# Optimization experiments

Hardware: AMD Instinct MI355X
Metric: run time of the kernel (lower is better)

## Reference

```python
import jax, jax.numpy as jnp
import numpy as np

N, W, D, IC, OC, R = 256, 1, 64, 32, 32, 8


def setup_inputs() -> dict:
    key = jax.random.key(0)
    k1, k2 = jax.random.split(key)
    x = jax.random.normal(k1, (N, W, D, IC, R), dtype=jnp.float32)
    weights = jax.random.normal(k2, (D, IC, OC, R), dtype=jnp.float32)
    return {"x": x, "weights": weights}


def reference(x, weights):
    # x: [n, w, d, ic, r] -> [n, w, d, ic, 1, r]
    # weights: [d, ic, oc, r] -> broadcast as [1, 1, d, ic, oc, r]
    # out: logsumexp over ic -> [n, w, d, oc, r]
    logits = x[:, :, :, :, None, :] + weights[None, None]
    return jax.nn.logsumexp(logits, axis=3)
```

## Files before the change

### kernel.cpp

```cpp
#include <hip/hip_runtime.h>
#include <hip/hip_bf16.h>


typedef __attribute__((ext_vector_type(8))) short bf16x8;
typedef __attribute__((ext_vector_type(4))) float f32x4;

constexpr int kD = 64, kIC = 32, kOC = 32, kR = 8;

__device__ __forceinline__ unsigned pk2(float a, float b) {
    __hip_bfloat162 h = __float22bfloat162_rn(make_float2(a, b));
    unsigned r;
    __builtin_memcpy(&r, &h, 4);
    return r;
}

__global__ __launch_bounds__(256) void lse_kernel(
    const float* __restrict__ x, const float* __restrict__ w,
    float* __restrict__ out)
{
    __shared__ __align__(16) unsigned short wsm[2 * 8 * 64 * 8];
    __shared__ __align__(16) unsigned short xs [8 * 64 * 8];

    const int t  = threadIdx.x;
    const int d  = blockIdx.x;
    const int n0 = blockIdx.y * 16;

    const int cw = t & 7, chw = cw & 1, cqw = cw >> 1, ol = t >> 3;
    const float* wd = w + (size_t)d * (kIC * kOC * kR);
    float4 wv[8];
    #pragma unroll
    for (int a = 0; a < 4; ++a) {
        const int ic0 = 8 * a + 2 * cqw;
        wv[2*a]   = *reinterpret_cast<const float4*>(wd + (size_t)ic0 * 256 + ol * 8 + 4 * chw);
        wv[2*a+1] = *reinterpret_cast<const float4*>(wd + (size_t)(ic0 + 1) * 256 + ol * 8 + 4 * chw);
    }

    const int cx = t & 15, e = cx & 1, icp = cx >> 1, nlx = t >> 4;
    const float* xr = x + (size_t)(n0 + nlx) * (kD * kIC * kR) + (size_t)d * (kIC * kR);
    float4 xv[4];
    #pragma unroll
    for (int a = 0; a < 2; ++a) {
        const int ic0 = 16 * a + 2 * icp;
        xv[2*a]   = *reinterpret_cast<const float4*>(xr + ic0 * 8 + 4 * e);
        xv[2*a+1] = *reinterpret_cast<const float4*>(xr + ic0 * 8 + 8 + 4 * e);
    }

    {
        const int col = ol & 15, u = ol >> 4, s0 = 2 * cqw;
        #pragma unroll
        for (int a = 0; a < 4; ++a)
            #pragma unroll
            for (int j = 0; j < 4; ++j) {
                const int r = 4 * chw + j;
                const unsigned pk = pk2(
                    __expf(reinterpret_cast<const float*>(&wv[2*a])[j]),
                    __expf(reinterpret_cast<const float*>(&wv[2*a+1])[j]));
                *reinterpret_cast<unsigned*>(&wsm[((u * 8 + r) * 64 + a * 16 + col) * 8 + s0]) = pk;
            }
    }

    {
        const int ig_lo = icp >> 2;
        const int s0x = 2 * (icp & 3);
        #pragma unroll
        for (int a = 0; a < 2; ++a) {
            const int lane = (2 * a + ig_lo) * 16 + nlx;
            #pragma unroll
            for (int j = 0; j < 4; ++j) {
                const int r = 4 * e + j;
                const unsigned pk = pk2(
                    __expf(reinterpret_cast<const float*>(&xv[2*a])[j]),
                    __expf(reinterpret_cast<const float*>(&xv[2*a+1])[j]));
                *reinterpret_cast<unsigned*>(&xs[(r * 64 + lane) * 8 + s0x]) = pk;
            }
        }
    }

    __syncthreads();

    const int wave = t >> 6;
    const int wu  = wave & 1;
    const int wrh = wave >> 1;
    const int l   = t & 63;
    const int colL = l & 15, qL = l >> 4;

    f32x4 acc[4];
    #pragma unroll
    for (int j = 0; j < 4; ++j) {
        const int r = wrh * 4 + j;
        bf16x8 av = *reinterpret_cast<const bf16x8*>(&xs [(r * 64 + l) * 8]);
        bf16x8 bv = *reinterpret_cast<const bf16x8*>(&wsm[((wu * 8 + r) * 64 + l) * 8]);
        f32x4 z = {0.f, 0.f, 0.f, 0.f};
        acc[j] = __builtin_amdgcn_mfma_f32_16x16x32_bf16(av, bv, z, 0, 0, 0);
    }

    #pragma unroll
    for (int i = 0; i < 4; ++i) {
        const int n = n0 + qL * 4 + i;
        float4 v;
        v.x = __logf(acc[0][i]); v.y = __logf(acc[1][i]);
        v.z = __logf(acc[2][i]); v.w = __logf(acc[3][i]);
        *reinterpret_cast<float4*>(out + (size_t)n * (kD * kOC * kR)
            + (size_t)d * (kOC * kR) + (size_t)(wu * 16 + colL) * 8 + wrh * 4) = v;
    }
}

extern "C" void kernel_launch(void* const* d_in, const int* in_sizes, int n_in,
                              void* d_out, int out_size, void* d_ws, size_t ws_size,
                              hipStream_t stream) {
    const float* x = (const float*)d_in[0];
    const float* w = (const float*)d_in[1];
    float* out = (float*)d_out;
    dim3 grid(kD, 16);
    lse_kernel<<<grid, 256, 0, stream>>>(x, w, out);
}
```

Measured before the change: 12.75 us.

## Process two batch tiles per block, reusing staged weights and overlapping staging

Each block now covers 32 batch rows (two 16-row tiles) rather than 16, so the exp-transformed weight tile in shared memory is built once and used twice, and the grid is halved to 512 blocks. The second x tile is exponentiated and staged into a second shared buffer while the first tile's MFMA results are turned into logs and stored, giving some overlap. In exchange it needs more registers and shared memory per block and has fewer blocks to spread across the 256 CUs.

```diff
diff --git a/kernel.cpp b/kernel.cpp
--- a/kernel.cpp
+++ b/kernel.cpp
@@ -19,11 +19,12 @@
     float* __restrict__ out)
 {
     __shared__ __align__(16) unsigned short wsm[2 * 8 * 64 * 8];
-    __shared__ __align__(16) unsigned short xs [8 * 64 * 8];
+    __shared__ __align__(16) unsigned short xs [2 * 8 * 64 * 8];
 
     const int t  = threadIdx.x;
-    const int d  = blockIdx.x;
-    const int n0 = blockIdx.y * 16;
+    const int d  = blockIdx.x >> 3;
+    const int pp = blockIdx.x & 7;
+    const int n0 = pp * 32;
 
     const int cw = t & 7, chw = cw & 1, cqw = cw >> 1, ol = t >> 3;
     const float* wd = w + (size_t)d * (kIC * kOC * kR);
@@ -36,13 +37,16 @@
     }
 
     const int cx = t & 15, e = cx & 1, icp = cx >> 1, nlx = t >> 4;
-    const float* xr = x + (size_t)(n0 + nlx) * (kD * kIC * kR) + (size_t)d * (kIC * kR);
-    float4 xv[4];
+    const float* xr0 = x + (size_t)(n0 + nlx) * (kD * kIC * kR) + (size_t)d * (kIC * kR);
+    const float* xr1 = xr0 + (size_t)16 * (kD * kIC * kR);
+    float4 x0v[4], x1v[4];
     #pragma unroll
     for (int a = 0; a < 2; ++a) {
         const int ic0 = 16 * a + 2 * icp;
-        xv[2*a]   = *reinterpret_cast<const float4*>(xr + ic0 * 8 + 4 * e);
-        xv[2*a+1] = *reinterpret_cast<const float4*>(xr + ic0 * 8 + 8 + 4 * e);
+        x0v[2*a]   = *reinterpret_cast<const float4*>(xr0 + ic0 * 8 + 4 * e);
+        x0v[2*a+1] = *reinterpret_cast<const float4*>(xr0 + ic0 * 8 + 8 + 4 * e);
+        x1v[2*a]   = *reinterpret_cast<const float4*>(xr1 + ic0 * 8 + 4 * e);
+        x1v[2*a+1] = *reinterpret_cast<const float4*>(xr1 + ic0 * 8 + 8 + 4 * e);
     }
 
     {
@@ -59,9 +63,8 @@
             }
     }
 
-    {
-        const int ig_lo = icp >> 2;
-        const int s0x = 2 * (icp & 3);
+    const int ig_lo = icp >> 2, s0x = 2 * (icp & 3);
+    auto stage_x = [&](int buf, const float4* xcv) {
         #pragma unroll
         for (int a = 0; a < 2; ++a) {
             const int lane = (2 * a + ig_lo) * 16 + nlx;
@@ -69,13 +72,14 @@
             for (int j = 0; j < 4; ++j) {
                 const int r = 4 * e + j;
                 const unsigned pk = pk2(
-                    __expf(reinterpret_cast<const float*>(&xv[2*a])[j]),
-                    __expf(reinterpret_cast<const float*>(&xv[2*a+1])[j]));
-                *reinterpret_cast<unsigned*>(&xs[(r * 64 + lane) * 8 + s0x]) = pk;
+                    __expf(reinterpret_cast<const float*>(&xcv[2*a])[j]),
+                    __expf(reinterpret_cast<const float*>(&xcv[2*a+1])[j]));
+                *reinterpret_cast<unsigned*>(&xs[((buf * 8 + r) * 64 + lane) * 8 + s0x]) = pk;
             }
         }
-    }
+    };
 
+    stage_x(0, x0v);
     __syncthreads();
 
     const int wave = t >> 6;
@@ -84,25 +88,35 @@
     const int l   = t & 63;
     const int colL = l & 15, qL = l >> 4;
 
-    f32x4 acc[4];
-    #pragma unroll
-    for (int j = 0; j < 4; ++j) {
-        const int r = wrh * 4 + j;
-        bf16x8 av = *reinterpret_cast<const bf16x8*>(&xs [(r * 64 + l) * 8]);
-        bf16x8 bv = *reinterpret_cast<const bf16x8*>(&wsm[((wu * 8 + r) * 64 + l) * 8]);
-        f32x4 z = {0.f, 0.f, 0.f, 0.f};
-        acc[j] = __builtin_amdgcn_mfma_f32_16x16x32_bf16(av, bv, z, 0, 0, 0);
-    }
+    auto compute = [&](int buf, f32x4* acc) {
+        #pragma unroll
+        for (int j = 0; j < 4; ++j) {
+            const int r = wrh * 4 + j;
+            bf16x8 av = *reinterpret_cast<const bf16x8*>(&xs [((buf * 8 + r) * 64 + l) * 8]);
+            bf16x8 bv = *reinterpret_cast<const bf16x8*>(&wsm[((wu * 8 + r) * 64 + l) * 8]);
+            f32x4 z = {0.f, 0.f, 0.f, 0.f};
+            acc[j] = __builtin_amdgcn_mfma_f32_16x16x32_bf16(av, bv, z, 0, 0, 0);
+        }
+    };
+    auto logstore = [&](int nt0, const f32x4* acc) {
+        #pragma unroll
+        for (int i = 0; i < 4; ++i) {
+            const int n = nt0 + qL * 4 + i;
+            float4 v;
+            v.x = __logf(acc[0][i]); v.y = __logf(acc[1][i]);
+            v.z = __logf(acc[2][i]); v.w = __logf(acc[3][i]);
+            *reinterpret_cast<float4*>(out + (size_t)n * (kD * kOC * kR)
+                + (size_t)d * (kOC * kR) + (size_t)(wu * 16 + colL) * 8 + wrh * 4) = v;
+        }
+    };
 
-    #pragma unroll
-    for (int i = 0; i < 4; ++i) {
-        const int n = n0 + qL * 4 + i;
-        float4 v;
-        v.x = __logf(acc[0][i]); v.y = __logf(acc[1][i]);
-        v.z = __logf(acc[2][i]); v.w = __logf(acc[3][i]);
-        *reinterpret_cast<float4*>(out + (size_t)n * (kD * kOC * kR)
-            + (size_t)d * (kOC * kR) + (size_t)(wu * 16 + colL) * 8 + wrh * 4) = v;
-    }
+    f32x4 acc0[4], acc1[4];
+    compute(0, acc0);
+    stage_x(1, x1v);
+    logstore(n0, acc0);
+    __syncthreads();
+    compute(1, acc1);
+    logstore(n0 + 16, acc1);
 }
 
 extern "C" void kernel_launch(void* const* d_in, const int* in_sizes, int n_in,
@@ -111,6 +125,5 @@
     const float* x = (const float*)d_in[0];
     const float* w = (const float*)d_in[1];
     float* out = (float*)d_out;
-    dim3 grid(kD, 16);
-    lse_kernel<<<grid, 256, 0, stream>>>(x, w, out);
+    lse_kernel<<<dim3(kD * 8), 256, 0, stream>>>(x, w, out);
 }
```

Measured after the change: 14.07 us. 10.4% more time.
